# Kernel tuning notes

Hardware: AMD Instinct MI355X
Metric: run time of the kernel (lower is better)

## Reference

```python
import jax, jax.numpy as jnp
import numpy as np

VOCAB = 8192
NT = 10        # spike encoder n_timesteps
N = 2048       # n_neurons
CA3 = 2048     # hippocampus CA3 size
S = 1024       # seq_len / context_length
SPARSITY = 0.05
LR = 0.01      # learning_rate * association_strength


def setup_inputs() -> dict:
    key = jax.random.key(0)
    k1, k2, k3, k4, k5 = jax.random.split(key, 5)
    token_ids = jax.random.randint(k1, (1, S), 0, VOCAB)                      # [batch=1, seq]
    sdr_table = jax.random.uniform(k2, (VOCAB, NT, N), dtype=jnp.float32)     # SDR encoder table
    pos_enc = jax.random.uniform(k3, (S, NT, N), dtype=jnp.float32)           # oscillatory position spikes (pre-threshold)
    w_hippo = jax.random.normal(k4, (CA3, N), dtype=jnp.float32) / np.sqrt(N).astype(np.float32)
    assoc_w = jax.random.normal(k5, (CA3, CA3), dtype=jnp.float32) * 0.01     # WEIGHT_INIT_SCALE_RECURRENT gaussian
    return {"token_ids": token_ids, "sdr_table": sdr_table, "pos_enc": pos_enc,
            "w_hippo": w_hippo, "assoc_w": assoc_w}


def reference(token_ids, sdr_table, pos_enc, w_hippo, assoc_w):
    """encode_sequence(learn=True): spike-encode each token, modulate by position
    spikes, run hippocampus, and sequentially Hebbian-update association weights.
    Returns final association weight matrix [CA3, CA3]."""
    tok_spikes = (sdr_table[token_ids[0]] < SPARSITY).astype(jnp.float32)
    # Position spikes (as_spikes=True -> binary) -> [S, NT, N]
    pos_spikes = (pos_enc < SPARSITY).astype(jnp.float32)
    # combined_spikes = token * (1 + 0.5 * position); sum over timesteps -> [S, N]
    hippo_input = (tok_spikes * (1.0 + 0.5 * pos_spikes)).sum(axis=1)
    # Hippocampus CA3 spikes: linear projection + threshold -> binary pattern [S, CA3]
    ca3_patterns = (hippo_input @ w_hippo.T > 0.0).astype(jnp.float32)

    # Sequential Hebbian association learning: W += lr * outer(post, pre), row-renorm.
    def step(W, pre_post):
        pre, post = pre_post
        W = W + LR * jnp.outer(post, pre)
        norm = jnp.maximum(jnp.linalg.norm(W, axis=1, keepdims=True), 1.0)
        return W / norm, None

    W_final, _ = jax.lax.scan(step, assoc_w, (ca3_patterns[:-1], ca3_patterns[1:]))
    return W_final
```

## Files before the change

kernel.cpp:

```cpp
#include <hip/hip_runtime.h>
#include <hip/hip_bf16.h>

#define NT    10
#define NN    2048
#define CA3C  2048
#define SEQ   1024
#define SPARS 0.05f
#define LRC   0.01f

typedef float          f32x4  __attribute__((ext_vector_type(4)));
typedef short          bf16x8 __attribute__((ext_vector_type(8)));
typedef unsigned short u16x4  __attribute__((ext_vector_type(4)));
typedef unsigned short u16x8  __attribute__((ext_vector_type(8)));

__device__ __forceinline__ unsigned short f2bf(float f) {
    unsigned u = __float_as_uint(f);
    u += 0x7FFFu + ((u >> 16) & 1u);
    return (unsigned short)(u >> 16);
}
__device__ __forceinline__ float bf2f(unsigned short h) {
    return __uint_as_float(((unsigned)h) << 16);
}

__global__ __launch_bounds__(256) void k_hippo(const int* __restrict__ tok,
        const float* __restrict__ sdr, const float* __restrict__ pos,
        unsigned short* __restrict__ Hh, unsigned* __restrict__ cnt) {
    if (blockIdx.x == 0 && blockIdx.y == 0 && threadIdx.x == 0) *cnt = 0;
    int s = blockIdx.x;
    int n = (blockIdx.y * 256 + threadIdx.x) * 4;
    const float* sp = sdr + (long)tok[s] * (NT * NN) + n;
    const float* pp = pos + (long)s * (NT * NN) + n;
    float a0 = 0.f, a1 = 0.f, a2 = 0.f, a3 = 0.f;
    #pragma unroll
    for (int t = 0; t < NT; ++t) {
        float4 sv = *(const float4*)(sp + t * NN);
        float4 pv = *(const float4*)(pp + t * NN);
        if (sv.x < SPARS) a0 += (pv.x < SPARS) ? 1.5f : 1.0f;
        if (sv.y < SPARS) a1 += (pv.y < SPARS) ? 1.5f : 1.0f;
        if (sv.z < SPARS) a2 += (pv.z < SPARS) ? 1.5f : 1.0f;
        if (sv.w < SPARS) a3 += (pv.w < SPARS) ? 1.5f : 1.0f;
    }
    u16x4 o = { f2bf(a0), f2bf(a1), f2bf(a2), f2bf(a3) };
    *(u16x4*)(Hh + (long)s * NN + n) = o;
}

__device__ __forceinline__ void split8(const float* __restrict__ src,
        unsigned short* __restrict__ hi, unsigned short* __restrict__ lo, long blk) {
    long i = (blk * 256 + threadIdx.x) * 8;
    f32x4 x0 = *(const f32x4*)(src + i);
    f32x4 x1 = *(const f32x4*)(src + i + 4);
    float xs[8] = {x0.x, x0.y, x0.z, x0.w, x1.x, x1.y, x1.z, x1.w};
    u16x8 h, l;
    #pragma unroll
    for (int j = 0; j < 8; ++j) {
        unsigned short hb = f2bf(xs[j]);
        h[j] = hb;
        l[j] = f2bf(xs[j] - bf2f(hb));
    }
    *(u16x8*)(hi + i) = h;
    if (lo) *(u16x8*)(lo + i) = l;
}

__global__ __launch_bounds__(256) void k_splits(const float* __restrict__ w_hippo,
        unsigned short* __restrict__ Wh, unsigned short* __restrict__ Wl,
        const float* __restrict__ assoc, unsigned short* __restrict__ Sh) {
    long b = blockIdx.x;
    if (b < 2048) split8(w_hippo, Wh, Wl, b);
    else         split8(assoc, Sh, nullptr, b - 2048);
}

#define SPLIT_NONE 0
#define SPLIT_A    1
#define SPLIT_B    2

template<int MODE, int BN>
__global__ __launch_bounds__(256, 1) void k_mgemm(
        const unsigned short* __restrict__ A0, const unsigned short* __restrict__ A1,
        const unsigned short* __restrict__ Bh, const unsigned short* __restrict__ B1,
        float* __restrict__ C, int M, int N, int K,
        const float* __restrict__ Wadd, const float* __restrict__ af) {
    constexpr int NTW = BN / 32;
    constexpr int XR  = (MODE == SPLIT_A) ? 128 : BN;
    __shared__ unsigned short LA[128 * 70];
    __shared__ unsigned short LB[BN * 70];
    __shared__ unsigned short LX[(MODE == SPLIT_NONE) ? 70 : XR * 70];
    int tid = threadIdx.x, wid = tid >> 6, l = tid & 63;
    int m0 = blockIdx.y * 128, n0 = blockIdx.x * BN;
    int wr = wid >> 1, wc = wid & 1;
    int fr = l & 15, fk = l >> 4;
    f32x4 acc[4][NTW] = {};
    int srow = wid * 8 + (l >> 3);
    int scol = (l & 7) * 8;
    bf16x8 ra[4], rb[BN / 32], rx[XR / 32];
    #pragma unroll
    for (int i = 0; i < 4; ++i)
        ra[i] = *(const bf16x8*)(A0 + (long)(m0 + i * 32 + srow) * K + scol);
    #pragma unroll
    for (int i = 0; i < BN / 32; ++i)
        rb[i] = *(const bf16x8*)(Bh + (long)(n0 + i * 32 + srow) * K + scol);
    if (MODE == SPLIT_A)
        #pragma unroll
        for (int i = 0; i < XR / 32; ++i)
            rx[i] = *(const bf16x8*)(A1 + (long)(m0 + i * 32 + srow) * K + scol);
    if (MODE == SPLIT_B)
        #pragma unroll
        for (int i = 0; i < XR / 32; ++i)
            rx[i] = *(const bf16x8*)(B1 + (long)(n0 + i * 32 + srow) * K + scol);

    for (int k0 = 0; k0 < K; k0 += 64) {
        __syncthreads();
        #pragma unroll
        for (int i = 0; i < 4; ++i) *(bf16x8*)&LA[(i * 32 + srow) * 70 + scol] = ra[i];
        #pragma unroll
        for (int i = 0; i < BN / 32; ++i) *(bf16x8*)&LB[(i * 32 + srow) * 70 + scol] = rb[i];
        if (MODE != SPLIT_NONE)
            #pragma unroll
            for (int i = 0; i < XR / 32; ++i) *(bf16x8*)&LX[(i * 32 + srow) * 70 + scol] = rx[i];
        __syncthreads();
        if (k0 + 64 < K) {
            int kn = k0 + 64;
            #pragma unroll
            for (int i = 0; i < 4; ++i)
                ra[i] = *(const bf16x8*)(A0 + (long)(m0 + i * 32 + srow) * K + kn + scol);
            #pragma unroll
            for (int i = 0; i < BN / 32; ++i)
                rb[i] = *(const bf16x8*)(Bh + (long)(n0 + i * 32 + srow) * K + kn + scol);
            if (MODE == SPLIT_A)
                #pragma unroll
                for (int i = 0; i < XR / 32; ++i)
                    rx[i] = *(const bf16x8*)(A1 + (long)(m0 + i * 32 + srow) * K + kn + scol);
            if (MODE == SPLIT_B)
                #pragma unroll
                for (int i = 0; i < XR / 32; ++i)
                    rx[i] = *(const bf16x8*)(B1 + (long)(n0 + i * 32 + srow) * K + kn + scol);
        }
        #pragma unroll
        for (int ks = 0; ks < 2; ++ks) {
            bf16x8 av[4], bv[NTW], xv[4];
            #pragma unroll
            for (int t = 0; t < 4; ++t)
                av[t] = *(const bf16x8*)&LA[(wr * 64 + t * 16 + fr) * 70 + ks * 32 + fk * 8];
            #pragma unroll
            for (int t = 0; t < NTW; ++t)
                bv[t] = *(const bf16x8*)&LB[(wc * (BN / 2) + t * 16 + fr) * 70 + ks * 32 + fk * 8];
            if (MODE == SPLIT_A)
                #pragma unroll
                for (int t = 0; t < 4; ++t)
                    xv[t] = *(const bf16x8*)&LX[(wr * 64 + t * 16 + fr) * 70 + ks * 32 + fk * 8];
            if (MODE == SPLIT_B)
                #pragma unroll
                for (int t = 0; t < NTW; ++t)
                    xv[t] = *(const bf16x8*)&LX[(wc * (BN / 2) + t * 16 + fr) * 70 + ks * 32 + fk * 8];
            #pragma unroll
            for (int mt = 0; mt < 4; ++mt)
                #pragma unroll
                for (int nt = 0; nt < NTW; ++nt) {
                    acc[mt][nt] = __builtin_amdgcn_mfma_f32_16x16x32_bf16(av[mt], bv[nt], acc[mt][nt], 0, 0, 0);
                    if (MODE == SPLIT_A)
                        acc[mt][nt] = __builtin_amdgcn_mfma_f32_16x16x32_bf16(xv[mt], bv[nt], acc[mt][nt], 0, 0, 0);
                    if (MODE == SPLIT_B)
                        acc[mt][nt] = __builtin_amdgcn_mfma_f32_16x16x32_bf16(av[mt], xv[nt], acc[mt][nt], 0, 0, 0);
                }
        }
    }
    int drb = (l >> 4) * 4;
    #pragma unroll
    for (int mt = 0; mt < 4; ++mt)
        #pragma unroll
        for (int nt = 0; nt < NTW; ++nt)
            #pragma unroll
            for (int e = 0; e < 4; ++e) {
                int row = m0 + wr * 64 + mt * 16 + drb + e;
                int cc  = n0 + wc * (BN / 2) + nt * 16 + (l & 15);
                float v = acc[mt][nt][e];
                if (Wadd) v = fmaf(af[row], Wadd[(long)row * N + cc], v);
                C[(long)row * N + cc] = v;
            }
}

__global__ __launch_bounds__(256) void k_fixflag(const float* __restrict__ dots,
        unsigned* __restrict__ list, unsigned* __restrict__ cnt) {
    int i = blockIdx.x * 256 + threadIdx.x;
    int lane = threadIdx.x & 63;
    bool f = fabsf(dots[i]) < 1e-3f;
    unsigned long long m = __ballot(f);
    if (m == 0) return;
    unsigned b0 = 0;
    if (lane == 0) b0 = atomicAdd(cnt, (unsigned)__popcll(m));
    b0 = __shfl(b0, 0, 64);
    if (f) {
        unsigned rank = (unsigned)__popcll(m & ((1ull << lane) - 1ull));
        list[b0 + rank] = (unsigned)i;
    }
}

__global__ __launch_bounds__(64) void k_fix64(const unsigned* __restrict__ list,
        const unsigned* __restrict__ cnt, const unsigned short* __restrict__ Hh,
        const float* __restrict__ w, float* __restrict__ dots) {
    int lane = threadIdx.x;
    unsigned n = *cnt;
    for (unsigned idx = blockIdx.x; idx < n; idx += gridDim.x) {
        unsigned i = list[idx];
        int s = (int)(i >> 11), c = (int)(i & 2047);
        const unsigned short* hr = Hh + (long)s * NN;
        const float* wr = w + (long)c * NN;
        double a = 0.0;
        #pragma unroll
        for (int j = 0; j < 8; ++j) {
            int k = j * 256 + lane * 4;
            f32x4 wv = *(const f32x4*)(wr + k);
            u16x4 hv = *(const u16x4*)(hr + k);
            a += (double)bf2f(hv.x) * (double)wv.x + (double)bf2f(hv.y) * (double)wv.y
               + (double)bf2f(hv.z) * (double)wv.z + (double)bf2f(hv.w) * (double)wv.w;
        }
        #pragma unroll
        for (int o = 1; o < 64; o <<= 1) a += __shfl_xor(a, o, 64);
        if (lane == 0) dots[i] = (a > 0.0) ? 1.0f : -1.0f;
    }
}

__global__ __launch_bounds__(256) void k_packx(const float* __restrict__ dots,
        unsigned* __restrict__ preT, float* __restrict__ popf,
        unsigned short* __restrict__ Xb, unsigned* __restrict__ postT) {
    int wid = threadIdx.x >> 6, lane = threadIdx.x & 63;
    if (blockIdx.x < 256) {
        int s = blockIdx.x * 4 + wid;
        const float* row = dots + (long)s * CA3C + lane * 32;
        unsigned short* xrow = Xb + (long)s * CA3C + lane * 32;
        unsigned m = 0;
        #pragma unroll
        for (int j4 = 0; j4 < 8; ++j4) {
            f32x4 v = *(const f32x4*)(row + j4 * 4);
            u16x4 xb;
            xb.x = v.x > 0.f ? 0x3F80 : 0; xb.y = v.y > 0.f ? 0x3F80 : 0;
            xb.z = v.z > 0.f ? 0x3F80 : 0; xb.w = v.w > 0.f ? 0x3F80 : 0;
            m |= (v.x > 0.f ? 1u : 0u) << (j4 * 4 + 0);
            m |= (v.y > 0.f ? 1u : 0u) << (j4 * 4 + 1);
            m |= (v.z > 0.f ? 1u : 0u) << (j4 * 4 + 2);
            m |= (v.w > 0.f ? 1u : 0u) << (j4 * 4 + 3);
            *(u16x4*)(xrow + j4 * 4) = xb;
        }
        preT[lane * SEQ + s] = m;
        int pc = __popc(m);
        #pragma unroll
        for (int o = 1; o < 64; o <<= 1) pc += __shfl_xor(pc, o, 64);
        if (lane == 0) popf[s] = (float)pc;
    } else {
        __shared__ unsigned long long masks[4][64];
        int tile = (blockIdx.x - 256) * 4 + wid;
        int rg = tile & 31, sg = tile >> 5;
        int r0 = rg * 64;
        #pragma unroll 8
        for (int k = 0; k < 64; ++k) {
            int s = sg * 64 + k;
            float d = (s < SEQ - 1) ? dots[(long)(s + 1) * CA3C + r0 + lane] : -1.f;
            unsigned long long m = __ballot(d > 0.f);
            if (lane == 0) masks[wid][k] = m;
        }
        unsigned w0 = 0, w1 = 0;
        #pragma unroll
        for (int k = 0; k < 32; ++k) {
            w0 |= (unsigned)((masks[wid][k]      >> lane) & 1ull) << k;
            w1 |= (unsigned)((masks[wid][k + 32] >> lane) & 1ull) << k;
        }
        postT[(r0 + lane) * 32 + sg * 2]     = w0;
        postT[(r0 + lane) * 32 + sg * 2 + 1] = w1;
    }
}

__global__ __launch_bounds__(256) void k_transpose(const unsigned short* __restrict__ Xb,
        unsigned short* __restrict__ XbT) {
    __shared__ unsigned short t[64][72];
    int s0 = blockIdx.x * 64, n0 = blockIdx.y * 64;
    int tx = threadIdx.x & 63, ty = threadIdx.x >> 6;
    #pragma unroll
    for (int ii = 0; ii < 16; ++ii) {
        int i = ty + ii * 4;
        t[i][tx] = Xb[(long)(s0 + i) * CA3C + n0 + tx];
    }
    __syncthreads();
    #pragma unroll
    for (int ii = 0; ii < 16; ++ii) {
        int i = ty + ii * 4;
        XbT[(long)(n0 + i) * SEQ + s0 + tx] = t[tx][i];
    }
}

__global__ __launch_bounds__(256) void k_gram(const unsigned* __restrict__ preT,
        float* __restrict__ G, unsigned short* __restrict__ Gbh,
        unsigned short* __restrict__ Gbl) {
    int i = blockIdx.x;
    int t = threadIdx.x;
    int a0 = 0, a1 = 0, a2 = 0, a3 = 0;
    #pragma unroll 8
    for (int w = 0; w < 64; ++w) {
        unsigned ri = preT[w * SEQ + i];
        const unsigned* pr = preT + w * SEQ;
        a0 += __popc(ri & pr[t]);
        a1 += __popc(ri & pr[t + 256]);
        a2 += __popc(ri & pr[t + 512]);
        a3 += __popc(ri & pr[t + 768]);
    }
    long base = (long)i * SEQ;
    int vi[4] = {a0, a1, a2, a3};
    #pragma unroll
    for (int q = 0; q < 4; ++q) {
        long o = base + t + q * 256;
        float v = (float)vi[q];
        unsigned short h = f2bf(v);
        G[o] = v;
        Gbh[o] = h;
        Gbl[o] = f2bf(v - bf2f(h));
    }
}

__device__ __forceinline__ float wave_sum64(float x) {
    #define DPPADD(ctrl, rmask) \
        x += __int_as_float(__builtin_amdgcn_update_dpp(0, __float_as_int(x), ctrl, rmask, 0xF, true))
    DPPADD(0xB1, 0xF);
    DPPADD(0x4E, 0xF);
    DPPADD(0x141, 0xF);
    DPPADD(0x140, 0xF);
    DPPADD(0x142, 0xA);
    DPPADD(0x143, 0xC);
    #undef DPPADD
    return __int_as_float(__builtin_amdgcn_readlane(__float_as_int(x), 63));
}

__global__ __launch_bounds__(256) void k_scan2(const float* __restrict__ W0,
        const float* __restrict__ B0, const float* __restrict__ G,
        const unsigned short* __restrict__ Gbh, const unsigned short* __restrict__ Gbl,
        const unsigned* __restrict__ postT, const float* __restrict__ popf,
        unsigned short* __restrict__ Ch, unsigned short* __restrict__ Cl,
        float* __restrict__ alphaf) {
    __shared__ float Gd[64][68];
    __shared__ unsigned short BH[2][4096];
    __shared__ unsigned short BL[2][4096];
    __shared__ unsigned short CHL[8][1024];
    int tid = threadIdx.x, wid = tid >> 6, lane = tid & 63;
    int r = blockIdx.x * 4 + wid;
    int fr = lane & 15, fk = lane >> 4;
    int nl = tid >> 2, seg = tid & 3;
    const float* wr = W0 + (long)r * NN + lane * 32;
    f32x4 q0 = *(const f32x4*)(wr +  0), q1 = *(const f32x4*)(wr +  4);
    f32x4 q2 = *(const f32x4*)(wr +  8), q3 = *(const f32x4*)(wr + 12);
    f32x4 q4 = *(const f32x4*)(wr + 16), q5 = *(const f32x4*)(wr + 20);
    f32x4 q6 = *(const f32x4*)(wr + 24), q7 = *(const f32x4*)(wr + 28);
    f32x4 pp = q0*q0 + q1*q1 + q2*q2 + q3*q3 + q4*q4 + q5*q5 + q6*q6 + q7*q7;
    float nu = wave_sum64((pp.x + pp.y) + (pp.z + pp.w));
    float alpha = 1.f, inv_alpha = 1.f;
    { float t = fmaxf(nu, 1.f); alpha *= rsqrtf(t); inv_alpha *= sqrtf(t); nu = fminf(nu, 1.f); }
    float s0 = 1.f;

    bf16x8 ph0, ph1, pl0, pl1;
    for (int b = 0; b < 16; ++b) {
        __syncthreads();
        {
            const float* gs = G + (long)(b * 64 + nl) * SEQ + b * 64 + seg * 16;
            *(f32x4*)&Gd[nl][seg * 16 +  0] = *(const f32x4*)(gs +  0);
            *(f32x4*)&Gd[nl][seg * 16 +  4] = *(const f32x4*)(gs +  4);
            *(f32x4*)&Gd[nl][seg * 16 +  8] = *(const f32x4*)(gs +  8);
            *(f32x4*)&Gd[nl][seg * 16 + 12] = *(const f32x4*)(gs + 12);
        }
        if (b > 0) {
            const unsigned short* gh = Gbh + (long)(b * 64 + nl) * SEQ + seg * 16;
            const unsigned short* gl = Gbl + (long)(b * 64 + nl) * SEQ + seg * 16;
            ph0 = *(const bf16x8*)(gh); ph1 = *(const bf16x8*)(gh + 8);
            pl0 = *(const bf16x8*)(gl); pl1 = *(const bf16x8*)(gl + 8);
            *(bf16x8*)&BH[0][((seg * 2 + 0) * 64 + nl) * 8] = ph0;
            *(bf16x8*)&BH[0][((seg * 2 + 1) * 64 + nl) * 8] = ph1;
            *(bf16x8*)&BL[0][((seg * 2 + 0) * 64 + nl) * 8] = pl0;
            *(bf16x8*)&BL[0][((seg * 2 + 1) * 64 + nl) * 8] = pl1;
        }
        __syncthreads();
        f32x4 acc0 = {}, acc1 = {}, acc2 = {}, acc3 = {};
        for (int ch = 0; ch < b; ++ch) {
            if (ch + 1 < b) {
                const unsigned short* gh = Gbh + (long)(b * 64 + nl) * SEQ + (ch + 1) * 64 + seg * 16;
                const unsigned short* gl = Gbl + (long)(b * 64 + nl) * SEQ + (ch + 1) * 64 + seg * 16;
                ph0 = *(const bf16x8*)(gh); ph1 = *(const bf16x8*)(gh + 8);
                pl0 = *(const bf16x8*)(gl); pl1 = *(const bf16x8*)(gl + 8);
            }
            const unsigned short* bh = BH[ch & 1];
            const unsigned short* bl = BL[ch & 1];
            #pragma unroll
            for (int kt = 0; kt < 2; ++kt) {
                bf16x8 af = *(const bf16x8*)&CHL[fr & 7][ch * 64 + kt * 32 + fk * 8];
                #define MTILE(T, ACC) { \
                    bf16x8 vh = *(const bf16x8*)&bh[((kt * 4 + fk) * 64 + T * 16 + fr) * 8]; \
                    bf16x8 vl = *(const bf16x8*)&bl[((kt * 4 + fk) * 64 + T * 16 + fr) * 8]; \
                    ACC = __builtin_amdgcn_mfma_f32_16x16x32_bf16(af, vh, ACC, 0, 0, 0); \
                    ACC = __builtin_amdgcn_mfma_f32_16x16x32_bf16(af, vl, ACC, 0, 0, 0); }
                MTILE(0, acc0) MTILE(1, acc1) MTILE(2, acc2) MTILE(3, acc3)
                #undef MTILE
            }
            if (ch + 1 < b) {
                int nb = (ch + 1) & 1;
                *(bf16x8*)&BH[nb][((seg * 2 + 0) * 64 + nl) * 8] = ph0;
                *(bf16x8*)&BH[nb][((seg * 2 + 1) * 64 + nl) * 8] = ph1;
                *(bf16x8*)&BL[nb][((seg * 2 + 0) * 64 + nl) * 8] = pl0;
                *(bf16x8*)&BL[nb][((seg * 2 + 1) * 64 + nl) * 8] = pl1;
            }
            __syncthreads();
        }
        float t0 = (wid & 1) ? (acc0.z + acc0.w) : (acc0.x + acc0.y);
        float t1 = (wid & 1) ? (acc1.z + acc1.w) : (acc1.x + acc1.y);
        float t2 = (wid & 1) ? (acc2.z + acc2.w) : (acc2.x + acc2.y);
        float t3 = (wid & 1) ? (acc3.z + acc3.w) : (acc3.x + acc3.y);
        int sa = (((wid >> 1) * 16) + fr) * 4;
        float p0 = __int_as_float(__builtin_amdgcn_ds_bpermute(sa, __float_as_int(t0)));
        float p1 = __int_as_float(__builtin_amdgcn_ds_bpermute(sa, __float_as_int(t1)));
        float p2 = __int_as_float(__builtin_amdgcn_ds_bpermute(sa, __float_as_int(t2)));
        float p3 = __int_as_float(__builtin_amdgcn_ds_bpermute(sa, __float_as_int(t3)));
        float u = (fk == 0) ? p0 : (fk == 1) ? p1 : (fk == 2) ? p2 : p3;

        float myB0  = B0[(long)r * SEQ + b * 64 + lane];
        float mypop = popf[b * 64 + lane];
        unsigned long long pm;
        {   unsigned lo = postT[r * 32 + 2 * b], hi = postT[r * 32 + 2 * b + 1];
            pm = ((unsigned long long)(unsigned)__builtin_amdgcn_readfirstlane((int)hi) << 32)
               |  (unsigned long long)(unsigned)__builtin_amdgcn_readfirstlane((int)lo);
        }
        float dacc = fmaf(s0, myB0, u);
        float cj = 0.f;
        #pragma unroll
        for (int j = 0; j < 64; ++j) {
            if ((pm >> j) & 1ull) {
                float dot = __int_as_float(__builtin_amdgcn_readlane(__float_as_int(dacc), j));
                float pj  = __int_as_float(__builtin_amdgcn_readlane(__float_as_int(mypop), j));
                float c = LRC * inv_alpha;
                nu = fmaf(2.f * LRC, alpha * dot, fmaf(LRC * LRC, pj, nu));
                float t = fmaxf(nu, 1.f);
                alpha *= rsqrtf(t); inv_alpha *= sqrtf(t); nu = fminf(nu, 1.f);
                dacc = fmaf(c, Gd[j][lane], dacc);
                cj = (lane == j) ? c : cj;
            }
        }
        {   unsigned short hh = f2bf(cj);
            CHL[wid * 2 + 0][b * 64 + lane] = hh;
            CHL[wid * 2 + 1][b * 64 + lane] = f2bf(cj - bf2f(hh));
        }
        if (inv_alpha > 1e10f) {
            #pragma unroll 1
            for (int kk = 0; kk <= b; ++kk) {
                float v = (bf2f(CHL[wid * 2 + 0][kk * 64 + lane])
                         + bf2f(CHL[wid * 2 + 1][kk * 64 + lane])) * alpha;
                unsigned short hh = f2bf(v);
                CHL[wid * 2 + 0][kk * 64 + lane] = hh;
                CHL[wid * 2 + 1][kk * 64 + lane] = f2bf(v - bf2f(hh));
            }
            s0 *= alpha; alpha = 1.f; inv_alpha = 1.f;
        }
    }
    if (lane == 0) alphaf[r] = alpha * s0;
    #pragma unroll
    for (int kk = 0; kk < 16; ++kk) {
        float v = (bf2f(CHL[wid * 2 + 0][kk * 64 + lane])
                 + bf2f(CHL[wid * 2 + 1][kk * 64 + lane])) * alpha;
        unsigned short hh = f2bf(v);
        Ch[(long)r * SEQ + kk * 64 + lane] = hh;
        Cl[(long)r * SEQ + kk * 64 + lane] = f2bf(v - bf2f(hh));
    }
}

extern "C" void kernel_launch(void* const* d_in, const int* in_sizes, int n_in,
                              void* d_out, int out_size, void* d_ws, size_t ws_size,
                              hipStream_t stream) {
    const int*   tok     = (const int*)d_in[0];
    const float* sdr     = (const float*)d_in[1];
    const float* pos     = (const float*)d_in[2];
    const float* w_hippo = (const float*)d_in[3];
    const float* assoc   = (const float*)d_in[4];
    float* out = (float*)d_out;

    char* ws = (char*)d_ws;
    unsigned short* Hh  = (unsigned short*)(ws);
    float*          G   = (float*)(ws);
    unsigned short* Wh  = (unsigned short*)(ws + (4l << 20));
    unsigned short* Wl  = (unsigned short*)(ws + (12l << 20));
    float*          dots= (float*)(ws + (20l << 20));
    float*          B0f = dots;
    unsigned short* Xb  = (unsigned short*)(ws + (28l << 20));
    unsigned short* Gbh = Xb;
    unsigned short* Gbl = (unsigned short*)(ws + (30l << 20));
    unsigned short* XbT = (unsigned short*)(ws + (32l << 20));
    unsigned* preT   = (unsigned*)(ws + (36l << 20));
    unsigned* postT  = (unsigned*)(ws + (36l << 20) + 262144);
    float*    popf   = (float*)(ws + (36l << 20) + 524288);
    float*    alphaf = (float*)(ws + (36l << 20) + 532480);
    unsigned* cnt    = (unsigned*)(ws + (37l << 20));
    unsigned* list   = (unsigned*)(ws + (37l << 20) + 4096);
    unsigned short* Sh  = (unsigned short*)(ws + (40l << 20));
    unsigned short* Ch  = (unsigned short*)(ws + (48l << 20));
    unsigned short* Cl  = (unsigned short*)(ws + (52l << 20));

    k_hippo                <<<dim3(SEQ, 2), 256, 0, stream>>>(tok, sdr, pos, Hh, cnt);
    k_splits               <<<4096,         256, 0, stream>>>(w_hippo, Wh, Wl, assoc, Sh);
    k_mgemm<SPLIT_B, 64>   <<<dim3(32, 8),  256, 0, stream>>>(Hh, nullptr, Wh, Wl, dots,
                                                              1024, 2048, 2048, nullptr, nullptr);
    k_fixflag              <<<8192,         256, 0, stream>>>(dots, list, cnt);
    k_fix64                <<<2048,          64, 0, stream>>>(list, cnt, Hh, w_hippo, dots);
    k_packx                <<<384,          256, 0, stream>>>(dots, preT, popf, Xb, postT);
    k_transpose            <<<dim3(16, 32), 256, 0, stream>>>(Xb, XbT);
    k_mgemm<SPLIT_NONE, 64><<<dim3(16, 16), 256, 0, stream>>>(Sh, nullptr, Xb, nullptr, B0f,
                                                              2048, 1024, 2048, nullptr, nullptr);
    k_gram                 <<<SEQ,          256, 0, stream>>>(preT, G, Gbh, Gbl);
    k_scan2                <<<512,          256, 0, stream>>>(assoc, B0f, G, Gbh, Gbl,
                                                              postT, popf, Ch, Cl, alphaf);
    k_mgemm<SPLIT_A, 128>  <<<dim3(16, 16), 256, 0, stream>>>(Ch, Cl, XbT, nullptr, out,
                                                              2048, 2048, 1024, assoc, alphaf);
}
```

Measured before the change: 464.9 us.

## Fuse pipeline kernels and shrink GEMM tiles to 64x64 for more blocks

Merges the hippo encode and weight split kernels into one launch. Folds the near-zero flagging into the first GEMM's epilogue, and combines the middle GEMM, transpose and gram kernels into one heterogeneous launch. All GEMMs switch to 64x64 tiles with two blocks per CU, so more blocks fill the GPU. This cuts launch count and a full pass over the dots buffer, but the smaller tiles lower data reuse and the epilogue atomics add contention. Gbh/Gbl move to their own buffers so they no longer alias Xb, which would otherwise be overwritten while k_mid reads Xb.

```diff
diff --git a/kernel.cpp b/kernel.cpp
--- a/kernel.cpp
+++ b/kernel.cpp
@@ -20,28 +20,6 @@
 }
 __device__ __forceinline__ float bf2f(unsigned short h) {
     return __uint_as_float(((unsigned)h) << 16);
-}
-
-__global__ __launch_bounds__(256) void k_hippo(const int* __restrict__ tok,
-        const float* __restrict__ sdr, const float* __restrict__ pos,
-        unsigned short* __restrict__ Hh, unsigned* __restrict__ cnt) {
-    if (blockIdx.x == 0 && blockIdx.y == 0 && threadIdx.x == 0) *cnt = 0;
-    int s = blockIdx.x;
-    int n = (blockIdx.y * 256 + threadIdx.x) * 4;
-    const float* sp = sdr + (long)tok[s] * (NT * NN) + n;
-    const float* pp = pos + (long)s * (NT * NN) + n;
-    float a0 = 0.f, a1 = 0.f, a2 = 0.f, a3 = 0.f;
-    #pragma unroll
-    for (int t = 0; t < NT; ++t) {
-        float4 sv = *(const float4*)(sp + t * NN);
-        float4 pv = *(const float4*)(pp + t * NN);
-        if (sv.x < SPARS) a0 += (pv.x < SPARS) ? 1.5f : 1.0f;
-        if (sv.y < SPARS) a1 += (pv.y < SPARS) ? 1.5f : 1.0f;
-        if (sv.z < SPARS) a2 += (pv.z < SPARS) ? 1.5f : 1.0f;
-        if (sv.w < SPARS) a3 += (pv.w < SPARS) ? 1.5f : 1.0f;
-    }
-    u16x4 o = { f2bf(a0), f2bf(a1), f2bf(a2), f2bf(a3) };
-    *(u16x4*)(Hh + (long)s * NN + n) = o;
 }
 
 __device__ __forceinline__ void split8(const float* __restrict__ src,
@@ -61,100 +39,97 @@
     if (lo) *(u16x8*)(lo + i) = l;
 }
 
-__global__ __launch_bounds__(256) void k_splits(const float* __restrict__ w_hippo,
-        unsigned short* __restrict__ Wh, unsigned short* __restrict__ Wl,
-        const float* __restrict__ assoc, unsigned short* __restrict__ Sh) {
-    long b = blockIdx.x;
-    if (b < 2048) split8(w_hippo, Wh, Wl, b);
-    else         split8(assoc, Sh, nullptr, b - 2048);
+__global__ __launch_bounds__(256) void k_front(const int* __restrict__ tok,
+        const float* __restrict__ sdr, const float* __restrict__ pos,
+        unsigned short* __restrict__ Hh, unsigned* __restrict__ cnt,
+        const float* __restrict__ w_hippo, unsigned short* __restrict__ Wh,
+        unsigned short* __restrict__ Wl, const float* __restrict__ assoc,
+        unsigned short* __restrict__ Sh) {
+    long id = blockIdx.x;
+    if (id == 0 && threadIdx.x == 0) *cnt = 0;
+    if (id < 2048) {
+        int s = (int)(id >> 1);
+        int n = ((int)(id & 1) * 256 + threadIdx.x) * 4;
+        const float* sp = sdr + (long)tok[s] * (NT * NN) + n;
+        const float* pp = pos + (long)s * (NT * NN) + n;
+        float a0 = 0.f, a1 = 0.f, a2 = 0.f, a3 = 0.f;
+        #pragma unroll
+        for (int t = 0; t < NT; ++t) {
+            float4 sv = *(const float4*)(sp + t * NN);
+            float4 pv = *(const float4*)(pp + t * NN);
+            if (sv.x < SPARS) a0 += (pv.x < SPARS) ? 1.5f : 1.0f;
+            if (sv.y < SPARS) a1 += (pv.y < SPARS) ? 1.5f : 1.0f;
+            if (sv.z < SPARS) a2 += (pv.z < SPARS) ? 1.5f : 1.0f;
+            if (sv.w < SPARS) a3 += (pv.w < SPARS) ? 1.5f : 1.0f;
+        }
+        u16x4 o = { f2bf(a0), f2bf(a1), f2bf(a2), f2bf(a3) };
+        *(u16x4*)(Hh + (long)s * NN + n) = o;
+    } else {
+        long b = id - 2048;
+        if (b < 2048) split8(w_hippo, Wh, Wl, b);
+        else          split8(assoc, Sh, nullptr, b - 2048);
+    }
 }
 
 #define SPLIT_NONE 0
 #define SPLIT_A    1
 #define SPLIT_B    2
 
-template<int MODE, int BN>
-__global__ __launch_bounds__(256, 1) void k_mgemm(
+template<int MODE, int FLAG>
+__device__ __forceinline__ void gemm64_body(int bx, int by,
         const unsigned short* __restrict__ A0, const unsigned short* __restrict__ A1,
         const unsigned short* __restrict__ Bh, const unsigned short* __restrict__ B1,
         float* __restrict__ C, int M, int N, int K,
-        const float* __restrict__ Wadd, const float* __restrict__ af) {
-    constexpr int NTW = BN / 32;
-    constexpr int XR  = (MODE == SPLIT_A) ? 128 : BN;
-    __shared__ unsigned short LA[128 * 70];
-    __shared__ unsigned short LB[BN * 70];
-    __shared__ unsigned short LX[(MODE == SPLIT_NONE) ? 70 : XR * 70];
+        const float* __restrict__ Wadd, const float* __restrict__ af,
+        unsigned* __restrict__ list, unsigned* __restrict__ cnt,
+        unsigned short* LA, unsigned short* LB, unsigned short* LX) {
     int tid = threadIdx.x, wid = tid >> 6, l = tid & 63;
-    int m0 = blockIdx.y * 128, n0 = blockIdx.x * BN;
+    int m0 = by * 64, n0 = bx * 64;
     int wr = wid >> 1, wc = wid & 1;
     int fr = l & 15, fk = l >> 4;
-    f32x4 acc[4][NTW] = {};
-    int srow = wid * 8 + (l >> 3);
-    int scol = (l & 7) * 8;
-    bf16x8 ra[4], rb[BN / 32], rx[XR / 32];
-    #pragma unroll
-    for (int i = 0; i < 4; ++i)
-        ra[i] = *(const bf16x8*)(A0 + (long)(m0 + i * 32 + srow) * K + scol);
-    #pragma unroll
-    for (int i = 0; i < BN / 32; ++i)
-        rb[i] = *(const bf16x8*)(Bh + (long)(n0 + i * 32 + srow) * K + scol);
-    if (MODE == SPLIT_A)
-        #pragma unroll
-        for (int i = 0; i < XR / 32; ++i)
-            rx[i] = *(const bf16x8*)(A1 + (long)(m0 + i * 32 + srow) * K + scol);
-    if (MODE == SPLIT_B)
-        #pragma unroll
-        for (int i = 0; i < XR / 32; ++i)
-            rx[i] = *(const bf16x8*)(B1 + (long)(n0 + i * 32 + srow) * K + scol);
-
+    f32x4 acc[2][2] = {};
+    int srow = tid >> 2, sc0 = (tid & 3) * 8;
+    bf16x8 ra[2], rb[2], rx[2];
+    #pragma unroll
+    for (int i = 0; i < 2; ++i) {
+        ra[i] = *(const bf16x8*)(A0 + (long)(m0 + srow) * K + sc0 + i * 32);
+        rb[i] = *(const bf16x8*)(Bh + (long)(n0 + srow) * K + sc0 + i * 32);
+        if (MODE == SPLIT_A) rx[i] = *(const bf16x8*)(A1 + (long)(m0 + srow) * K + sc0 + i * 32);
+        if (MODE == SPLIT_B) rx[i] = *(const bf16x8*)(B1 + (long)(n0 + srow) * K + sc0 + i * 32);
+    }
     for (int k0 = 0; k0 < K; k0 += 64) {
         __syncthreads();
         #pragma unroll
-        for (int i = 0; i < 4; ++i) *(bf16x8*)&LA[(i * 32 + srow) * 70 + scol] = ra[i];
-        #pragma unroll
-        for (int i = 0; i < BN / 32; ++i) *(bf16x8*)&LB[(i * 32 + srow) * 70 + scol] = rb[i];
-        if (MODE != SPLIT_NONE)
-            #pragma unroll
-            for (int i = 0; i < XR / 32; ++i) *(bf16x8*)&LX[(i * 32 + srow) * 70 + scol] = rx[i];
+        for (int i = 0; i < 2; ++i) {
+            *(bf16x8*)&LA[srow * 70 + sc0 + i * 32] = ra[i];
+            *(bf16x8*)&LB[srow * 70 + sc0 + i * 32] = rb[i];
+            if (MODE != SPLIT_NONE) *(bf16x8*)&LX[srow * 70 + sc0 + i * 32] = rx[i];
+        }
         __syncthreads();
         if (k0 + 64 < K) {
             int kn = k0 + 64;
             #pragma unroll
-            for (int i = 0; i < 4; ++i)
-                ra[i] = *(const bf16x8*)(A0 + (long)(m0 + i * 32 + srow) * K + kn + scol);
+            for (int i = 0; i < 2; ++i) {
+                ra[i] = *(const bf16x8*)(A0 + (long)(m0 + srow) * K + kn + sc0 + i * 32);
+                rb[i] = *(const bf16x8*)(Bh + (long)(n0 + srow) * K + kn + sc0 + i * 32);
+                if (MODE == SPLIT_A) rx[i] = *(const bf16x8*)(A1 + (long)(m0 + srow) * K + kn + sc0 + i * 32);
+                if (MODE == SPLIT_B) rx[i] = *(const bf16x8*)(B1 + (long)(n0 + srow) * K + kn + sc0 + i * 32);
+            }
+        }
+        #pragma unroll
+        for (int ks = 0; ks < 2; ++ks) {
+            bf16x8 av[2], bv[2], xv[2];
             #pragma unroll
-            for (int i = 0; i < BN / 32; ++i)
-                rb[i] = *(const bf16x8*)(Bh + (long)(n0 + i * 32 + srow) * K + kn + scol);
-            if (MODE == SPLIT_A)
+            for (int t = 0; t < 2; ++t) {
+                av[t] = *(const bf16x8*)&LA[(wr * 32 + t * 16 + fr) * 70 + ks * 32 + fk * 8];
+                bv[t] = *(const bf16x8*)&LB[(wc * 32 + t * 16 + fr) * 70 + ks * 32 + fk * 8];
+                if (MODE == SPLIT_A) xv[t] = *(const bf16x8*)&LX[(wr * 32 + t * 16 + fr) * 70 + ks * 32 + fk * 8];
+                if (MODE == SPLIT_B) xv[t] = *(const bf16x8*)&LX[(wc * 32 + t * 16 + fr) * 70 + ks * 32 + fk * 8];
+            }
+            #pragma unroll
+            for (int mt = 0; mt < 2; ++mt)
                 #pragma unroll
-                for (int i = 0; i < XR / 32; ++i)
-                    rx[i] = *(const bf16x8*)(A1 + (long)(m0 + i * 32 + srow) * K + kn + scol);
-            if (MODE == SPLIT_B)
-                #pragma unroll
-                for (int i = 0; i < XR / 32; ++i)
-                    rx[i] = *(const bf16x8*)(B1 + (long)(n0 + i * 32 + srow) * K + kn + scol);
-        }
-        #pragma unroll
-        for (int ks = 0; ks < 2; ++ks) {
-            bf16x8 av[4], bv[NTW], xv[4];
-            #pragma unroll
-            for (int t = 0; t < 4; ++t)
-                av[t] = *(const bf16x8*)&LA[(wr * 64 + t * 16 + fr) * 70 + ks * 32 + fk * 8];
-            #pragma unroll
-            for (int t = 0; t < NTW; ++t)
-                bv[t] = *(const bf16x8*)&LB[(wc * (BN / 2) + t * 16 + fr) * 70 + ks * 32 + fk * 8];
-            if (MODE == SPLIT_A)
-                #pragma unroll
-                for (int t = 0; t < 4; ++t)
-                    xv[t] = *(const bf16x8*)&LX[(wr * 64 + t * 16 + fr) * 70 + ks * 32 + fk * 8];
-            if (MODE == SPLIT_B)
-                #pragma unroll
-                for (int t = 0; t < NTW; ++t)
-                    xv[t] = *(const bf16x8*)&LX[(wc * (BN / 2) + t * 16 + fr) * 70 + ks * 32 + fk * 8];
-            #pragma unroll
-            for (int mt = 0; mt < 4; ++mt)
-                #pragma unroll
-                for (int nt = 0; nt < NTW; ++nt) {
+                for (int nt = 0; nt < 2; ++nt) {
                     acc[mt][nt] = __builtin_amdgcn_mfma_f32_16x16x32_bf16(av[mt], bv[nt], acc[mt][nt], 0, 0, 0);
                     if (MODE == SPLIT_A)
                         acc[mt][nt] = __builtin_amdgcn_mfma_f32_16x16x32_bf16(xv[mt], bv[nt], acc[mt][nt], 0, 0, 0);
@@ -165,33 +140,44 @@
     }
     int drb = (l >> 4) * 4;
     #pragma unroll
-    for (int mt = 0; mt < 4; ++mt)
-        #pragma unroll
-        for (int nt = 0; nt < NTW; ++nt)
+    for (int mt = 0; mt < 2; ++mt)
+        #pragma unroll
+        for (int nt = 0; nt < 2; ++nt)
             #pragma unroll
             for (int e = 0; e < 4; ++e) {
-                int row = m0 + wr * 64 + mt * 16 + drb + e;
-                int cc  = n0 + wc * (BN / 2) + nt * 16 + (l & 15);
+                int row = m0 + wr * 32 + mt * 16 + drb + e;
+                int cc  = n0 + wc * 32 + nt * 16 + (l & 15);
                 float v = acc[mt][nt][e];
                 if (Wadd) v = fmaf(af[row], Wadd[(long)row * N + cc], v);
                 C[(long)row * N + cc] = v;
-            }
-}
-
-__global__ __launch_bounds__(256) void k_fixflag(const float* __restrict__ dots,
+                if (FLAG) {
+                    bool f = fabsf(v) < 1e-3f;
+                    unsigned long long mb = __ballot(f);
+                    if (mb) {
+                        unsigned base = 0;
+                        if (l == 0) base = atomicAdd(cnt, (unsigned)__popcll(mb));
+                        base = __shfl(base, 0, 64);
+                        if (f) {
+                            unsigned rank = (unsigned)__popcll(mb & ((1ull << l) - 1ull));
+                            list[base + rank] = (unsigned)((long)row * N + cc);
+                        }
+                    }
+                }
+            }
+}
+
+template<int MODE, int FLAG>
+__global__ __launch_bounds__(256, 2) void k_gemm64(
+        const unsigned short* __restrict__ A0, const unsigned short* __restrict__ A1,
+        const unsigned short* __restrict__ Bh, const unsigned short* __restrict__ B1,
+        float* __restrict__ C, int M, int N, int K,
+        const float* __restrict__ Wadd, const float* __restrict__ af,
         unsigned* __restrict__ list, unsigned* __restrict__ cnt) {
-    int i = blockIdx.x * 256 + threadIdx.x;
-    int lane = threadIdx.x & 63;
-    bool f = fabsf(dots[i]) < 1e-3f;
-    unsigned long long m = __ballot(f);
-    if (m == 0) return;
-    unsigned b0 = 0;
-    if (lane == 0) b0 = atomicAdd(cnt, (unsigned)__popcll(m));
-    b0 = __shfl(b0, 0, 64);
-    if (f) {
-        unsigned rank = (unsigned)__popcll(m & ((1ull << lane) - 1ull));
-        list[b0 + rank] = (unsigned)i;
-    }
+    __shared__ unsigned short LA[64 * 70];
+    __shared__ unsigned short LB[64 * 70];
+    __shared__ unsigned short LX[(MODE == SPLIT_NONE) ? 70 : 64 * 70];
+    gemm64_body<MODE, FLAG>(blockIdx.x, blockIdx.y, A0, A1, Bh, B1, C, M, N, K,
+                            Wadd, af, list, cnt, LA, LB, LX);
 }
 
 __global__ __launch_bounds__(64) void k_fix64(const unsigned* __restrict__ list,
@@ -268,28 +254,26 @@
     }
 }
 
-__global__ __launch_bounds__(256) void k_transpose(const unsigned short* __restrict__ Xb,
-        unsigned short* __restrict__ XbT) {
-    __shared__ unsigned short t[64][72];
-    int s0 = blockIdx.x * 64, n0 = blockIdx.y * 64;
+__device__ __forceinline__ void transpose_body(int t, const unsigned short* __restrict__ Xb,
+        unsigned short* __restrict__ XbT, unsigned short (*sm)[72]) {
+    int s0 = (t & 15) * 64, n0 = (t >> 4) * 64;
     int tx = threadIdx.x & 63, ty = threadIdx.x >> 6;
     #pragma unroll
     for (int ii = 0; ii < 16; ++ii) {
         int i = ty + ii * 4;
-        t[i][tx] = Xb[(long)(s0 + i) * CA3C + n0 + tx];
+        sm[i][tx] = Xb[(long)(s0 + i) * CA3C + n0 + tx];
     }
     __syncthreads();
     #pragma unroll
     for (int ii = 0; ii < 16; ++ii) {
         int i = ty + ii * 4;
-        XbT[(long)(n0 + i) * SEQ + s0 + tx] = t[tx][i];
-    }
-}
-
-__global__ __launch_bounds__(256) void k_gram(const unsigned* __restrict__ preT,
+        XbT[(long)(n0 + i) * SEQ + s0 + tx] = sm[tx][i];
+    }
+}
+
+__device__ __forceinline__ void gram_body(int i, const unsigned* __restrict__ preT,
         float* __restrict__ G, unsigned short* __restrict__ Gbh,
         unsigned short* __restrict__ Gbl) {
-    int i = blockIdx.x;
     int t = threadIdx.x;
     int a0 = 0, a1 = 0, a2 = 0, a3 = 0;
     #pragma unroll 8
@@ -311,6 +295,24 @@
         G[o] = v;
         Gbh[o] = h;
         Gbl[o] = f2bf(v - bf2f(h));
+    }
+}
+
+__global__ __launch_bounds__(256, 2) void k_mid(const unsigned short* __restrict__ Sh,
+        const unsigned short* __restrict__ Xb, float* __restrict__ B0f,
+        const unsigned* __restrict__ preT, float* __restrict__ G,
+        unsigned short* __restrict__ Gbh, unsigned short* __restrict__ Gbl,
+        unsigned short* __restrict__ XbT) {
+    __shared__ unsigned short smem[2 * 64 * 70];
+    int id = blockIdx.x;
+    if (id < 512) {
+        gemm64_body<SPLIT_NONE, 0>(id & 15, id >> 4, Sh, nullptr, Xb, nullptr, B0f,
+                                   2048, 1024, 2048, nullptr, nullptr, nullptr, nullptr,
+                                   smem, smem + 64 * 70, smem);
+    } else if (id < 1024) {
+        transpose_body(id - 512, Xb, XbT, (unsigned short (*)[72])smem);
+    } else {
+        gram_body(id - 1024, preT, G, Gbh, Gbl);
     }
 }
 
@@ -481,8 +483,6 @@
     float*          dots= (float*)(ws + (20l << 20));
     float*          B0f = dots;
     unsigned short* Xb  = (unsigned short*)(ws + (28l << 20));
-    unsigned short* Gbh = Xb;
-    unsigned short* Gbl = (unsigned short*)(ws + (30l << 20));
     unsigned short* XbT = (unsigned short*)(ws + (32l << 20));
     unsigned* preT   = (unsigned*)(ws + (36l << 20));
     unsigned* postT  = (unsigned*)(ws + (36l << 20) + 262144);
@@ -493,20 +493,20 @@
     unsigned short* Sh  = (unsigned short*)(ws + (40l << 20));
     unsigned short* Ch  = (unsigned short*)(ws + (48l << 20));
     unsigned short* Cl  = (unsigned short*)(ws + (52l << 20));
-
-    k_hippo                <<<dim3(SEQ, 2), 256, 0, stream>>>(tok, sdr, pos, Hh, cnt);
-    k_splits               <<<4096,         256, 0, stream>>>(w_hippo, Wh, Wl, assoc, Sh);
-    k_mgemm<SPLIT_B, 64>   <<<dim3(32, 8),  256, 0, stream>>>(Hh, nullptr, Wh, Wl, dots,
-                                                              1024, 2048, 2048, nullptr, nullptr);
-    k_fixflag              <<<8192,         256, 0, stream>>>(dots, list, cnt);
-    k_fix64                <<<2048,          64, 0, stream>>>(list, cnt, Hh, w_hippo, dots);
-    k_packx                <<<384,          256, 0, stream>>>(dots, preT, popf, Xb, postT);
-    k_transpose            <<<dim3(16, 32), 256, 0, stream>>>(Xb, XbT);
-    k_mgemm<SPLIT_NONE, 64><<<dim3(16, 16), 256, 0, stream>>>(Sh, nullptr, Xb, nullptr, B0f,
-                                                              2048, 1024, 2048, nullptr, nullptr);
-    k_gram                 <<<SEQ,          256, 0, stream>>>(preT, G, Gbh, Gbl);
-    k_scan2                <<<512,          256, 0, stream>>>(assoc, B0f, G, Gbh, Gbl,
-                                                              postT, popf, Ch, Cl, alphaf);
-    k_mgemm<SPLIT_A, 128>  <<<dim3(16, 16), 256, 0, stream>>>(Ch, Cl, XbT, nullptr, out,
-                                                              2048, 2048, 1024, assoc, alphaf);
-}
+    unsigned short* Gbh = (unsigned short*)(ws + (56l << 20));
+    unsigned short* Gbl = (unsigned short*)(ws + (58l << 20));
+
+    k_front               <<<6144,         256, 0, stream>>>(tok, sdr, pos, Hh, cnt,
+                                                             w_hippo, Wh, Wl, assoc, Sh);
+    k_gemm64<SPLIT_B, 1>  <<<dim3(32, 16), 256, 0, stream>>>(Hh, nullptr, Wh, Wl, dots,
+                                                             1024, 2048, 2048, nullptr, nullptr,
+                                                             list, cnt);
+    k_fix64               <<<2048,          64, 0, stream>>>(list, cnt, Hh, w_hippo, dots);
+    k_packx               <<<384,          256, 0, stream>>>(dots, preT, popf, Xb, postT);
+    k_mid                 <<<2048,         256, 0, stream>>>(Sh, Xb, B0f, preT, G, Gbh, Gbl, XbT);
+    k_scan2               <<<512,          256, 0, stream>>>(assoc, B0f, G, Gbh, Gbl,
+                                                             postT, popf, Ch, Cl, alphaf);
+    k_gemm64<SPLIT_A, 0>  <<<dim3(32, 32), 256, 0, stream>>>(Ch, Cl, XbT, nullptr, out,
+                                                             2048, 2048, 1024, assoc, alphaf,
+                                                             nullptr, nullptr);
+}
```

Result: slower. 667.9 us (+43.7%).
